# Kernel optimization log

Hardware: AMD Instinct MI355X
Metric: run time of the kernel (lower is better)

## Reference

```python
import jax, jax.numpy as jnp
import numpy as np


def setup_inputs() -> dict:
    key = jax.random.key(0)
    k1, k2, k3 = jax.random.split(key, 3)
    N, Q, K, E = 8, 2048, 2048, 512
    query = jax.random.normal(k1, (N, Q, E), dtype=jnp.float32)
    keys = jax.random.normal(k2, (N, K, E), dtype=jnp.float32)
    values = jax.random.normal(k3, (N, K, E), dtype=jnp.float32)
    return {"query": query, "keys": keys, "values": values}


def reference(query, keys, values):
    # energy: [N, Q, K] -- note: NO 1/sqrt(d) scaling, matching the original
    energy = jnp.einsum('nqe,nke->nqk', query, keys)
    attention = jax.nn.softmax(energy, axis=-1)
    out = jnp.einsum('nqk,nke->nqe', attention, values)
    return out
```

## Files before the change

kernel.cpp:

```cpp
#include <hip/hip_runtime.h>
#include <stdint.h>


typedef __attribute__((ext_vector_type(8))) _Float16 half8;
typedef __attribute__((ext_vector_type(2))) _Float16 half2;
typedef __attribute__((ext_vector_type(4))) float    floatx4;

#define NBATCH 8
#define SEQ    2048
#define EDIM   512
static constexpr size_t NE = (size_t)NBATCH * SEQ * EDIM;

__device__ __forceinline__ void block_sync_lds() {
  asm volatile("s_waitcnt lgkmcnt(0)\n\ts_barrier" ::: "memory");
}


__global__ void make_frags(const float* __restrict__ q, const float* __restrict__ k,
                           const float* __restrict__ v,
                           _Float16* __restrict__ qf, _Float16* __restrict__ kf,
                           _Float16* __restrict__ vf) {
  const int tid = threadIdx.x;
  if (blockIdx.x < 2048) {
#pragma unroll
    for (int i = 0; i < 4; i++) {
      const uint32_t c = blockIdx.x * 1024u + i * 256u + tid;
      const uint32_t ln = c & 63u, idx = c >> 6;
      const uint32_t est = idx & 15u, rt = (idx >> 4) & 127u;
      const uint32_t n = (idx >> 11) & 7u, tensor = idx >> 14;
      const float* src = (tensor ? k : q) +
          ((size_t)(n * SEQ + rt * 16 + (ln & 15u))) * EDIM + est * 32 + (ln >> 4) * 8;
      float4 a = *reinterpret_cast<const float4*>(src);
      float4 b = *reinterpret_cast<const float4*>(src + 4);
      half8 h;
      h[0] = (_Float16)a.x; h[1] = (_Float16)a.y; h[2] = (_Float16)a.z; h[3] = (_Float16)a.w;
      h[4] = (_Float16)b.x; h[5] = (_Float16)b.y; h[6] = (_Float16)b.z; h[7] = (_Float16)b.w;
      *reinterpret_cast<half8*>((tensor ? kf : qf) + (size_t)(c & 0xFFFFFu) * 8) = h;
    }
  } else {
    __shared__ float lds[32][260];
    const int b2 = blockIdx.x - 2048;
    const int n = b2 >> 6, kt = b2 & 63;
    const float* src = v + ((size_t)n * SEQ + kt * 32) * EDIM;
    _Float16* dst = vf + ((size_t)(n * 64 + kt) * 32) * 512;
#pragma unroll
    for (int eh = 0; eh < 2; eh++) {
      if (eh) __syncthreads();
#pragma unroll
      for (int i = 0; i < 8; i++) {
        int c = i * 256 + tid;
        int row = c >> 6, col4 = c & 63;
        float4 x = *reinterpret_cast<const float4*>(src + (size_t)row * EDIM + eh * 256 + col4 * 4);
        *reinterpret_cast<float4*>(&lds[row][col4 * 4]) = x;
      }
      __syncthreads();
#pragma unroll
      for (int i = 0; i < 4; i++) {
        int fl = i * 256 + tid;
        int etl = fl >> 6, ln = fl & 63;
        int m15 = ln & 15, q4 = ln >> 4;
        int e_local = etl * 16 + m15;
        half8 h;
#pragma unroll
        for (int j = 0; j < 8; j++) h[j] = (_Float16)lds[q4 * 8 + j][e_local];
        *reinterpret_cast<half8*>(dst + ((size_t)eh * 1024 + fl) * 8) = h;
      }
    }
  }
}

__launch_bounds__(512, 4)
__global__ void attn_fused(const _Float16* __restrict__ qf, const _Float16* __restrict__ kf,
                           const _Float16* __restrict__ vf, float* __restrict__ out) {
  __shared__ float    s_part[4][32][36];
  __shared__ _Float16 p_lds[32][40];
  __shared__ float    m_lds[32], l_lds[32], a_lds[32];

  const int tid  = threadIdx.x;
  const int lane = tid & 63, w = tid >> 6;
  const int m15  = lane & 15, q4 = lane >> 4;
  const int n    = blockIdx.x & 7, qt = blockIdx.x >> 3;
  const int ks   = w & 1, es = w >> 1;

  if (tid < 32) { m_lds[tid] = -3.0e38f; l_lds[tid] = 0.0f; }

  half8 qfr[2][4];
  {
    const uint32_t qbase = ((uint32_t)(n * 128 + qt * 2) * 16 + es * 4) * 512 + (uint32_t)lane * 8;
#pragma unroll
    for (int s = 0; s < 2; s++)
#pragma unroll
      for (int i = 0; i < 4; i++)
        qfr[s][i] = *reinterpret_cast<const half8*>(qf + qbase + (uint32_t)(s * 16 + i) * 512);
  }

  floatx4 oacc[2][4];
#pragma unroll
  for (int s = 0; s < 2; s++)
#pragma unroll
    for (int j = 0; j < 4; j++) oacc[s][j] = (floatx4){0.f, 0.f, 0.f, 0.f};

  uint32_t koff = ((uint32_t)(n * 128 + ks) * 16 + es * 4) * 512 + (uint32_t)lane * 8;
  uint32_t voff = ((uint32_t)(n * 64) * 32 + w * 4) * 512 + (uint32_t)lane * 8;

  block_sync_lds();

  for (int t = 0; t < 64; t++) {
    half8 kfr[4];
#pragma unroll
    for (int i = 0; i < 4; i++)
      kfr[i] = *reinterpret_cast<const half8*>(kf + koff + (uint32_t)i * 512);
    koff += 16384;

    floatx4 sacc[2];
    sacc[0] = (floatx4){0.f, 0.f, 0.f, 0.f};
    sacc[1] = (floatx4){0.f, 0.f, 0.f, 0.f};
    __builtin_amdgcn_s_setprio(1);
#pragma unroll
    for (int i = 0; i < 4; i++) {
      sacc[0] = __builtin_amdgcn_mfma_f32_16x16x32_f16(qfr[0][i], kfr[i], sacc[0], 0, 0, 0);
      sacc[1] = __builtin_amdgcn_mfma_f32_16x16x32_f16(qfr[1][i], kfr[i], sacc[1], 0, 0, 0);
    }
    __builtin_amdgcn_s_setprio(0);

    half8 vfr[4];
#pragma unroll
    for (int j = 0; j < 4; j++)
      vfr[j] = *reinterpret_cast<const half8*>(vf + voff + (uint32_t)j * 512);
    voff += 16384;

#pragma unroll
    for (int s = 0; s < 2; s++)
#pragma unroll
      for (int r = 0; r < 4; r++)
        s_part[es][s * 16 + q4 * 4 + r][ks * 16 + m15] = sacc[s][r];
    block_sync_lds();

    {
      const int r = tid >> 4, sub = tid & 15, c = sub * 2;
      float svx = s_part[0][r][c],     svy = s_part[0][r][c + 1];
#pragma unroll
      for (int pl = 1; pl < 4; pl++) { svx += s_part[pl][r][c]; svy += s_part[pl][r][c + 1]; }
      float mx = fmaxf(svx, svy);
#pragma unroll
      for (int o = 1; o < 16; o <<= 1) mx = fmaxf(mx, __shfl_xor(mx, o));
      const float mo = m_lds[r];
      const float mn = fmaxf(mo, mx);
      const float px = __expf(svx - mn), py = __expf(svy - mn);
      float rs = px + py;
#pragma unroll
      for (int o = 1; o < 16; o <<= 1) rs += __shfl_xor(rs, o);
      if (sub == 0) {
        const float al = __expf(mo - mn);
        a_lds[r] = al; m_lds[r] = mn; l_lds[r] = l_lds[r] * al + rs;
      }
      half2 ph; ph[0] = (_Float16)px; ph[1] = (_Float16)py;
      *reinterpret_cast<half2*>(&p_lds[r][c]) = ph;
    }
    block_sync_lds();

    half8 pfr[2];
    pfr[0] = *reinterpret_cast<const half8*>(&p_lds[m15][q4 * 8]);
    pfr[1] = *reinterpret_cast<const half8*>(&p_lds[16 + m15][q4 * 8]);
    {
      floatx4 al0 = *reinterpret_cast<floatx4*>(&a_lds[q4 * 4]);
      floatx4 al1 = *reinterpret_cast<floatx4*>(&a_lds[16 + q4 * 4]);
#pragma unroll
      for (int j = 0; j < 4; j++) { oacc[0][j] *= al0; oacc[1][j] *= al1; }
    }
    __builtin_amdgcn_s_setprio(1);
#pragma unroll
    for (int j = 0; j < 4; j++) {
      oacc[0][j] = __builtin_amdgcn_mfma_f32_16x16x32_f16(pfr[0], vfr[j], oacc[0][j], 0, 0, 0);
      oacc[1][j] = __builtin_amdgcn_mfma_f32_16x16x32_f16(pfr[1], vfr[j], oacc[1][j], 0, 0, 0);
    }
    __builtin_amdgcn_s_setprio(0);
  }

  const int q0 = qt * 32;
#pragma unroll
  for (int s = 0; s < 2; s++) {
    floatx4 lv = *reinterpret_cast<floatx4*>(&l_lds[s * 16 + q4 * 4]);
#pragma unroll
    for (int j = 0; j < 4; j++) {
      const int col = (w * 4 + j) * 16 + m15;
#pragma unroll
      for (int r = 0; r < 4; r++) {
        const int row = s * 16 + q4 * 4 + r;
        out[((size_t)n * SEQ + q0 + row) * EDIM + col] = oacc[s][j][r] / lv[r];
      }
    }
  }
}

__global__ void attn_fallback(const float* __restrict__ q, const float* __restrict__ k,
                              const float* __restrict__ v, float* __restrict__ out) {
  __shared__ float qrow[EDIM];
  __shared__ float sc[SEQ];
  __shared__ float red[16];
  const int tid = threadIdx.x;
  const int n = blockIdx.x >> 11, qi = blockIdx.x & 2047;
  const int wv = tid >> 6, ln = tid & 63;
  const float* qp = q + ((size_t)n * SEQ + qi) * EDIM;
  for (int e = tid; e < EDIM; e += 256) qrow[e] = qp[e];
  __syncthreads();
  for (int kk = wv; kk < SEQ; kk += 4) {
    const float* kp = k + ((size_t)n * SEQ + kk) * EDIM;
    float s = 0.f;
    for (int e = ln; e < EDIM; e += 64) s = fmaf(qrow[e], kp[e], s);
    for (int o = 32; o > 0; o >>= 1) s += __shfl_down(s, o);
    if (ln == 0) sc[kk] = s;
  }
  __syncthreads();
  float mx = -3.0e38f;
  for (int kk = tid; kk < SEQ; kk += 256) mx = fmaxf(mx, sc[kk]);
  for (int o = 32; o > 0; o >>= 1) mx = fmaxf(mx, __shfl_down(mx, o));
  if (ln == 0) red[wv] = mx;
  __syncthreads();
  if (tid == 0) {
    float m2 = red[0];
    for (int i = 1; i < 4; i++) m2 = fmaxf(m2, red[i]);
    red[8] = m2;
  }
  __syncthreads();
  const float m = red[8];
  float ls = 0.f;
  for (int kk = tid; kk < SEQ; kk += 256) { float p = __expf(sc[kk] - m); sc[kk] = p; ls += p; }
  for (int o = 32; o > 0; o >>= 1) ls += __shfl_down(ls, o);
  if (ln == 0) red[wv] = ls;
  __syncthreads();
  if (tid == 0) { red[9] = red[0] + red[1] + red[2] + red[3]; }
  __syncthreads();
  const float linv = 1.f / red[9];
  for (int e = tid; e < EDIM; e += 256) {
    float acc = 0.f;
    const float* vp = v + ((size_t)n * SEQ) * EDIM + e;
    for (int kk = 0; kk < SEQ; kk++) acc = fmaf(sc[kk], vp[(size_t)kk * EDIM], acc);
    out[((size_t)n * SEQ + qi) * EDIM + e] = acc * linv;
  }
}

extern "C" void kernel_launch(void* const* d_in, const int* in_sizes, int n_in,
                              void* d_out, int out_size, void* d_ws, size_t ws_size,
                              hipStream_t stream) {
  const float* q = (const float*)d_in[0];
  const float* k = (const float*)d_in[1];
  const float* v = (const float*)d_in[2];
  float* out = (float*)d_out;
  const size_t need = 3 * NE * sizeof(_Float16);
  if (ws_size >= need) {
    _Float16* qf = (_Float16*)d_ws;
    _Float16* kf = qf + NE;
    _Float16* vf = kf + NE;
    make_frags<<<2560, 256, 0, stream>>>(q, k, v, qf, kf, vf);
    attn_fused<<<512, 512, 0, stream>>>(qf, kf, vf, out);
  } else {
    attn_fallback<<<16384, 256, 0, stream>>>(q, k, v, out);
  }
}
```

Before: 235.5 us.

## Fuse Q/K fp16 conversion into attention kernel, keep only V pre-pack

Drops the separate pre-pass that converted Q and K to fp16 fragment layout. The attention kernel now loads fp32 Q and K straight from the inputs and converts them in registers, and only V is still repacked by a smaller kernel. This removes the write and re-read of two fp16 workspace tensors and shrinks the pre-pass. In exchange, each K tile is read as fp32, which doubles its bytes per read, and because K is reused by all 64 q-tile blocks per batch this adds load traffic and conversion work inside the main loop.

```diff
diff --git a/kernel.cpp b/kernel.cpp
--- a/kernel.cpp
+++ b/kernel.cpp
@@ -15,62 +15,48 @@
   asm volatile("s_waitcnt lgkmcnt(0)\n\ts_barrier" ::: "memory");
 }
 
-
-__global__ void make_frags(const float* __restrict__ q, const float* __restrict__ k,
-                           const float* __restrict__ v,
-                           _Float16* __restrict__ qf, _Float16* __restrict__ kf,
-                           _Float16* __restrict__ vf) {
+__device__ __forceinline__ half8 cvt8(float4 a, float4 b) {
+  half8 h;
+  h[0] = (_Float16)a.x; h[1] = (_Float16)a.y; h[2] = (_Float16)a.z; h[3] = (_Float16)a.w;
+  h[4] = (_Float16)b.x; h[5] = (_Float16)b.y; h[6] = (_Float16)b.z; h[7] = (_Float16)b.w;
+  return h;
+}
+
+
+__global__ void make_vfrags(const float* __restrict__ v, _Float16* __restrict__ vf) {
+  __shared__ float lds[32][260];
   const int tid = threadIdx.x;
-  if (blockIdx.x < 2048) {
+  const int b2 = blockIdx.x;
+  const int n = b2 >> 6, kt = b2 & 63;
+  const float* src = v + ((size_t)n * SEQ + kt * 32) * EDIM;
+  _Float16* dst = vf + ((size_t)(n * 64 + kt) * 32) * 512;
+#pragma unroll
+  for (int eh = 0; eh < 2; eh++) {
+    if (eh) __syncthreads();
+#pragma unroll
+    for (int i = 0; i < 8; i++) {
+      int c = i * 256 + tid;
+      int row = c >> 6, col4 = c & 63;
+      float4 x = *reinterpret_cast<const float4*>(src + (size_t)row * EDIM + eh * 256 + col4 * 4);
+      *reinterpret_cast<float4*>(&lds[row][col4 * 4]) = x;
+    }
+    __syncthreads();
 #pragma unroll
     for (int i = 0; i < 4; i++) {
-      const uint32_t c = blockIdx.x * 1024u + i * 256u + tid;
-      const uint32_t ln = c & 63u, idx = c >> 6;
-      const uint32_t est = idx & 15u, rt = (idx >> 4) & 127u;
-      const uint32_t n = (idx >> 11) & 7u, tensor = idx >> 14;
-      const float* src = (tensor ? k : q) +
-          ((size_t)(n * SEQ + rt * 16 + (ln & 15u))) * EDIM + est * 32 + (ln >> 4) * 8;
-      float4 a = *reinterpret_cast<const float4*>(src);
-      float4 b = *reinterpret_cast<const float4*>(src + 4);
+      int fl = i * 256 + tid;
+      int etl = fl >> 6, ln = fl & 63;
+      int m15 = ln & 15, q4 = ln >> 4;
+      int e_local = etl * 16 + m15;
       half8 h;
-      h[0] = (_Float16)a.x; h[1] = (_Float16)a.y; h[2] = (_Float16)a.z; h[3] = (_Float16)a.w;
-      h[4] = (_Float16)b.x; h[5] = (_Float16)b.y; h[6] = (_Float16)b.z; h[7] = (_Float16)b.w;
-      *reinterpret_cast<half8*>((tensor ? kf : qf) + (size_t)(c & 0xFFFFFu) * 8) = h;
-    }
-  } else {
-    __shared__ float lds[32][260];
-    const int b2 = blockIdx.x - 2048;
-    const int n = b2 >> 6, kt = b2 & 63;
-    const float* src = v + ((size_t)n * SEQ + kt * 32) * EDIM;
-    _Float16* dst = vf + ((size_t)(n * 64 + kt) * 32) * 512;
-#pragma unroll
-    for (int eh = 0; eh < 2; eh++) {
-      if (eh) __syncthreads();
-#pragma unroll
-      for (int i = 0; i < 8; i++) {
-        int c = i * 256 + tid;
-        int row = c >> 6, col4 = c & 63;
-        float4 x = *reinterpret_cast<const float4*>(src + (size_t)row * EDIM + eh * 256 + col4 * 4);
-        *reinterpret_cast<float4*>(&lds[row][col4 * 4]) = x;
-      }
-      __syncthreads();
-#pragma unroll
-      for (int i = 0; i < 4; i++) {
-        int fl = i * 256 + tid;
-        int etl = fl >> 6, ln = fl & 63;
-        int m15 = ln & 15, q4 = ln >> 4;
-        int e_local = etl * 16 + m15;
-        half8 h;
-#pragma unroll
-        for (int j = 0; j < 8; j++) h[j] = (_Float16)lds[q4 * 8 + j][e_local];
-        *reinterpret_cast<half8*>(dst + ((size_t)eh * 1024 + fl) * 8) = h;
-      }
+#pragma unroll
+      for (int j = 0; j < 8; j++) h[j] = (_Float16)lds[q4 * 8 + j][e_local];
+      *reinterpret_cast<half8*>(dst + ((size_t)eh * 1024 + fl) * 8) = h;
     }
   }
 }
 
 __launch_bounds__(512, 4)
-__global__ void attn_fused(const _Float16* __restrict__ qf, const _Float16* __restrict__ kf,
+__global__ void attn_fused(const float* __restrict__ q, const float* __restrict__ k,
                            const _Float16* __restrict__ vf, float* __restrict__ out) {
   __shared__ float    s_part[4][32][36];
   __shared__ _Float16 p_lds[32][40];
@@ -86,12 +72,16 @@
 
   half8 qfr[2][4];
   {
-    const uint32_t qbase = ((uint32_t)(n * 128 + qt * 2) * 16 + es * 4) * 512 + (uint32_t)lane * 8;
+    const float* qb = q + ((size_t)n * SEQ + qt * 32 + m15) * EDIM + es * 128 + q4 * 8;
 #pragma unroll
     for (int s = 0; s < 2; s++)
 #pragma unroll
-      for (int i = 0; i < 4; i++)
-        qfr[s][i] = *reinterpret_cast<const half8*>(qf + qbase + (uint32_t)(s * 16 + i) * 512);
+      for (int i = 0; i < 4; i++) {
+        const float* src = qb + (size_t)s * 16 * EDIM + i * 32;
+        float4 a = *reinterpret_cast<const float4*>(src);
+        float4 b = *reinterpret_cast<const float4*>(src + 4);
+        qfr[s][i] = cvt8(a, b);
+      }
   }
 
   floatx4 oacc[2][4];
@@ -100,17 +90,23 @@
 #pragma unroll
     for (int j = 0; j < 4; j++) oacc[s][j] = (floatx4){0.f, 0.f, 0.f, 0.f};
 
-  uint32_t koff = ((uint32_t)(n * 128 + ks) * 16 + es * 4) * 512 + (uint32_t)lane * 8;
+  uint32_t koff = ((uint32_t)(n * SEQ + ks * 16 + m15)) * EDIM + es * 128 + q4 * 8;
   uint32_t voff = ((uint32_t)(n * 64) * 32 + w * 4) * 512 + (uint32_t)lane * 8;
 
   block_sync_lds();
 
   for (int t = 0; t < 64; t++) {
+    float4 ka[4], kb[4];
+#pragma unroll
+    for (int i = 0; i < 4; i++) {
+      ka[i] = *reinterpret_cast<const float4*>(k + koff + (uint32_t)i * 32);
+      kb[i] = *reinterpret_cast<const float4*>(k + koff + (uint32_t)i * 32 + 4);
+    }
+    koff += 32u * EDIM;
+
     half8 kfr[4];
 #pragma unroll
-    for (int i = 0; i < 4; i++)
-      kfr[i] = *reinterpret_cast<const half8*>(kf + koff + (uint32_t)i * 512);
-    koff += 16384;
+    for (int i = 0; i < 4; i++) kfr[i] = cvt8(ka[i], kb[i]);
 
     floatx4 sacc[2];
     sacc[0] = (floatx4){0.f, 0.f, 0.f, 0.f};
@@ -247,13 +243,11 @@
   const float* k = (const float*)d_in[1];
   const float* v = (const float*)d_in[2];
   float* out = (float*)d_out;
-  const size_t need = 3 * NE * sizeof(_Float16);
+  const size_t need = NE * sizeof(_Float16);
   if (ws_size >= need) {
-    _Float16* qf = (_Float16*)d_ws;
-    _Float16* kf = qf + NE;
-    _Float16* vf = kf + NE;
-    make_frags<<<2560, 256, 0, stream>>>(q, k, v, qf, kf, vf);
-    attn_fused<<<512, 512, 0, stream>>>(qf, kf, vf, out);
+    _Float16* vf = (_Float16*)d_ws;
+    make_vfrags<<<512, 256, 0, stream>>>(v, vf);
+    attn_fused<<<512, 512, 0, stream>>>(q, k, vf, out);
   } else {
     attn_fallback<<<16384, 256, 0, stream>>>(q, k, v, out);
   }
```

Result: slower. 429.3 us (+82.3%).
